# Kernel tuning notes

Hardware: AMD Instinct MI355X
Metric: run time of the kernel (lower is better)

The kernel has to match this reference:

```python
import jax, jax.numpy as jnp
import numpy as np

B, T, H, W, C = 2, 8, 20, 36, 512
NH = 4
HD = C // NH
WS = (5, 9)
EXP = (2, 4)              # window_size // 2
KP = (5, 9)               # focal unfold kernel for level k=0
PADP = (2, 4)
T2T_K, T2T_S, T2T_P = (7, 7), (3, 3), (3, 3)
FFN_HD = 1960
NWH, NWW = H // WS[0], W // WS[1]   # 4, 4
WAREA = WS[0] * WS[1]               # 45


def _valid_ind_rolled():
    wh, ww = WS
    eh, ew = EXP
    m = np.ones((4, wh, ww), np.float32)
    m[0, :wh - eh, :ww - ew] = 0   # tl
    m[1, :wh - eh, ew:] = 0        # tr
    m[2, eh:, :ww - ew] = 0        # bl
    m[3, eh:, ew:] = 0             # br
    return jnp.asarray(np.nonzero(m.reshape(-1))[0])

VALID_ROLLED = _valid_ind_rolled()  # (120,)


def unfold(x, k, s, p):
    # x: (N, Cc, Hh, Ww) -> (N, Cc*kh*kw, L); matches torch.nn.Unfold layout (c slowest).
    N, Cc, Hh, Ww = x.shape
    kh, kw = k; sh, sw = s; ph, pw = p
    xp = jnp.pad(x, ((0, 0), (0, 0), (ph, ph), (pw, pw)))
    oh = (Hh + 2 * ph - kh) // sh + 1
    ow = (Ww + 2 * pw - kw) // sw + 1
    cols = [xp[:, :, i:i + oh * sh:sh, j:j + ow * sw:sw]
            for i in range(kh) for j in range(kw)]
    patches = jnp.stack(cols, axis=2)            # (N, Cc, kh*kw, oh, ow)
    return patches.reshape(N, Cc * kh * kw, oh * ow)


def fold(patches, out_hw, k, s, p):
    # inverse of unfold (overlap-add), matches torch F.fold.
    N = patches.shape[0]
    kh, kw = k; sh, sw = s; ph, pw = p
    Hh, Ww = out_hw
    oh = (Hh + 2 * ph - kh) // sh + 1
    ow = (Ww + 2 * pw - kw) // sw + 1
    Cc = patches.shape[1] // (kh * kw)
    pr = patches.reshape(N, Cc, kh, kw, oh, ow)
    out = jnp.zeros((N, Cc, Hh + 2 * ph, Ww + 2 * pw), patches.dtype)
    for i in range(kh):
        for j in range(kw):
            out = out.at[:, :, i:i + oh * sh:sh, j:j + ow * sw:sw].add(pr[:, :, i, j])
    return out[:, :, ph:ph + Hh, pw:pw + Ww]


def layer_norm(x, g, b):
    mu = jnp.mean(x, -1, keepdims=True)
    var = jnp.var(x, -1, keepdims=True)
    return (x - mu) * jax.lax.rsqrt(var + 1e-5) * g + b


def win_part(x):
    # (B,T,H,W,C) -> (B*nW, T*wh*ww, C)
    b = x.shape[0]
    x = x.reshape(b, T, NWH, WS[0], NWW, WS[1], C)
    return x.transpose(0, 2, 4, 1, 3, 5, 6).reshape(-1, T * WAREA, C)


def to_heads(w):
    return w.reshape(-1, T, WAREA, NH, HD).transpose(0, 3, 1, 2, 4).reshape(-1, NH, T * WAREA, HD)


def block_forward(x, g1, be1, wqkv, bqkv, wproj, bproj, wpool, bpool, g2, be2, w1, bf1, w2, bf2, out_h, out_w):
    shortcut = x
    xn = layer_norm(x, g1, be1)

    # ---- coarser (pooled) focal level, k=0 (focal_level=2) ----
    wnr = xn.reshape(B, T, NWH, WS[0], NWW, WS[1], C).transpose(0, 2, 4, 1, 3, 5, 6)
    wnr = wnr.reshape(B, NWH, NWW, T, WAREA, C)
    pooled = jnp.einsum('bhwtnc,n->bhwtc', wnr, wpool) + bpool   # (B,NWH,NWW,T,C)

    # ---- window attention ----
    qkv = xn @ wqkv + bqkv                                       # (B,T,H,W,3C)
    q, k, v = jnp.split(qkv, 3, axis=-1)
    qw = to_heads(win_part(q)) * (HD ** -0.5)
    kw_, vw = to_heads(win_part(k)), to_heads(win_part(v))

    def rolled(t):
        parts = []
        for sh, sw in ((-EXP[0], -EXP[1]), (-EXP[0], EXP[1]), (EXP[0], -EXP[1]), (EXP[0], EXP[1])):
            r = jnp.roll(t, (sh, sw), axis=(2, 3))
            parts.append(win_part(r).reshape(-1, T, WAREA, NH, HD))
        cat = jnp.concatenate(parts, axis=2)                     # (B*nW, T, 4*warea, NH, HD)
        cat = jnp.take(cat.transpose(0, 3, 1, 2, 4), VALID_ROLLED, axis=3)
        return cat.reshape(-1, NH, T * VALID_ROLLED.shape[0], HD)

    k_rolled = jnp.concatenate([kw_, rolled(k)], axis=2)         # (B*nW, NH, T*165, HD)
    v_rolled = jnp.concatenate([vw, rolled(v)], axis=2)

    # pooled keys/values via focal unfold
    xp = pooled.transpose(0, 3, 1, 2, 4)                          # (B,T,NWH,NWW,C)
    qkv_p = xp @ wqkv + bqkv
    kp, vp = qkv_p[..., C:2 * C], qkv_p[..., 2 * C:]

    def unfold_kv(t):
        t = t.transpose(0, 1, 4, 2, 3).reshape(B * T, C, NWH, NWW)
        u = unfold(t, KP, (1, 1), PADP)                           # (B*T, C*45, L)
        L = u.shape[-1]
        u = u.reshape(B, T, C, KP[0], KP[1], L).transpose(0, 5, 1, 3, 4, 2)
        u = u.reshape(B * L, T, KP[0] * KP[1], NH, HD).transpose(0, 3, 1, 2, 4)
        return u.reshape(B * L, NH, T * KP[0] * KP[1], HD)

    k_all = jnp.concatenate([k_rolled, unfold_kv(kp)], axis=2)
    v_all = jnp.concatenate([v_rolled, unfold_kv(vp)], axis=2)

    attn = jnp.einsum('wnqd,wnkd->wnqk', qw, k_all)               # (B*nW, NH, T*45, N)

    # validity mask for pooled context (zero-padded unfold positions -> -100)
    ones = jnp.ones((T, 1, NWH, NWW), x.dtype)
    um = unfold(ones, KP, (1, 1), PADP)                           # (T, 45, L)
    L = um.shape[-1]
    mvals = jnp.where(um.reshape(T, KP[0] * KP[1], L).transpose(2, 0, 1).reshape(L, -1) == 0,
                      jnp.asarray(-100.0, x.dtype), jnp.asarray(0.0, x.dtype))
    n_rolled = k_rolled.shape[2]
    mask_cols = jnp.concatenate([jnp.zeros((L, n_rolled), x.dtype), mvals], axis=1)
    attn = attn + jnp.tile(mask_cols, (B, 1))[:, None, None, :]

    attn = jax.nn.softmax(attn, axis=-1)
    out = jnp.einsum('wnqk,wnkd->wnqd', attn, v_all)
    out = out.transpose(0, 2, 1, 3).reshape(-1, T * WAREA, C) @ wproj + bproj

    # window reverse + residual
    out = out.reshape(B, NWH, NWW, T, WS[0], WS[1], C)
    out = out.transpose(0, 3, 1, 4, 2, 5, 6).reshape(B, T, H, W, C)
    x = shortcut + out

    # ---- FusionFeedForward (fold/unfold re-normalized MLP) ----
    y = layer_norm(x, g2, be2).reshape(B, T * H * W, C)
    h = y @ w1 + bf1                                              # (B, n, 1960)
    nvec = ((out_h + 2 * T2T_P[0] - T2T_K[0]) // T2T_S[0] + 1) * \
           ((out_w + 2 * T2T_P[1] - T2T_K[1]) // T2T_S[1] + 1)
    bt = (B * T * H * W) // nvec
    norm_p = jnp.ones((bt, T2T_K[0] * T2T_K[1], nvec), x.dtype)
    norm_f = fold(norm_p, (out_h, out_w), T2T_K, T2T_S, T2T_P)    # (bt,1,out_h,out_w)
    h_f = fold(h.reshape(bt, nvec, FFN_HD).transpose(0, 2, 1), (out_h, out_w), T2T_K, T2T_S, T2T_P)
    h = unfold(h_f / norm_f, T2T_K, T2T_S, T2T_P).transpose(0, 2, 1).reshape(B, T * H * W, FFN_HD)
    h = jax.nn.gelu(h, approximate=False) @ w2 + bf2
    return x + h.reshape(B, T, H, W, C)


def setup_inputs() -> dict:
    key = jax.random.key(0)
    ks = jax.random.split(key, 8)
    s = 0.02
    return dict(
        x=jax.random.normal(ks[0], (B, T, H, W, C), jnp.float32),
        g1=jnp.ones((C,), jnp.float32),
        be1=jnp.zeros((C,), jnp.float32),
        wqkv=jax.random.normal(ks[1], (C, 3 * C), jnp.float32) * s,
        bqkv=jnp.zeros((3 * C,), jnp.float32),
        wproj=jax.random.normal(ks[2], (C, C), jnp.float32) * s,
        bproj=jnp.zeros((C,), jnp.float32),
        wpool=jnp.full((WAREA,), 1.0 / WAREA, jnp.float32),
        bpool=jnp.zeros((1,), jnp.float32),
        g2=jnp.ones((C,), jnp.float32),
        be2=jnp.zeros((C,), jnp.float32),
        w1=jax.random.normal(ks[3], (C, FFN_HD), jnp.float32) * s,
        bf1=jnp.zeros((FFN_HD,), jnp.float32),
        w2=jax.random.normal(ks[4], (FFN_HD, C), jnp.float32) * s,
        bf2=jnp.zeros((C,), jnp.float32),
        out_h=60,
        out_w=108,
    )


def reference(x, g1, be1, wqkv, bqkv, wproj, bproj, wpool, bpool, g2, be2, w1, bf1, w2, bf2, out_h, out_w):
    return block_forward(x, g1, be1, wqkv, bqkv, wproj, bproj, wpool, bpool,
                         g2, be2, w1, bf1, w2, bf2, out_h, out_w)
```

## Files before the change

### kernel.cpp

```cpp
#include <hip/hip_runtime.h>
#include <hip/hip_bf16.h>
#include <math.h>

typedef __hip_bfloat16 bf16;
typedef __attribute__((ext_vector_type(8))) short bf16x8;
typedef __attribute__((ext_vector_type(4))) float f32x4;

#define DEVI __device__ __forceinline__

#define C_ 512
#define NH_ 4
#define NTOK 11520
#define NKEY 1680
#define NRK 120
#define FFN_ 1960
#define ZROW (NTOK + 256)

DEVI float ldf(const bf16* p) { return __bfloat162float(*p); }
DEVI float ldf(const float* p) { return *p; }
DEVI void stw(bf16* p, float v) { *p = __float2bfloat16(v); }
DEVI void stw(float* p, float v) { *p = v; }
DEVI unsigned short f2bs(float f) { bf16 h = __float2bfloat16(f); return *(unsigned short*)&h; }

template <int DT> DEVI float ldw(const void* p, size_t i) {
  if (DT == 0) return __bfloat162float(((const bf16*)p)[i]);
  else         return ((const float*)p)[i];
}

DEVI void gload_lds16(const void* g, void* l) {
  __builtin_amdgcn_global_load_lds(
      (const __attribute__((address_space(1))) void*)g,
      (__attribute__((address_space(3))) void*)l, 16, 0, 0);
}

__global__ void k_init(const void* __restrict__ g1, int* __restrict__ flag,
                       int* __restrict__ table, bf16* __restrict__ zp) {
  if (blockIdx.x == 0) {
    if (threadIdx.x == 0) {
      const unsigned short* p = (const unsigned short*)g1;
      *flag = (p[0] == 0x3F80u) ? 0 : 1;
      int cnt = 0;
      for (int pq = 0; pq < 4; pq++)
        for (int wi = 0; wi < 5; wi++)
          for (int wj = 0; wj < 9; wj++) {
            bool invalid;
            if (pq == 0)      invalid = (wi < 3) && (wj < 5);
            else if (pq == 1) invalid = (wi < 3) && (wj >= 4);
            else if (pq == 2) invalid = (wi >= 2) && (wj < 5);
            else              invalid = (wi >= 2) && (wj >= 4);
            if (!invalid) table[cnt++] = pq * 45 + wi * 9 + wj;
          }
    }
  } else {
    zp[(blockIdx.x - 1) * 256 + threadIdx.x] = __float2bfloat16(0.f);
  }
}

__global__ void k_ksrc(const int* __restrict__ vtab, int* __restrict__ ksrc) {
  int idx = blockIdx.x * 256 + threadIdx.x;
  if (idx >= 32 * NKEY) return;
  int w = idx / NKEY, j = idx % NKEY;
  int b = w >> 4, nh = (w >> 2) & 3, nw = w & 3;
  int val;
  if (j < 360) {
    int t = j / 45, pos = j % 45, wi = pos / 9, wj2 = pos % 9;
    val = ((b * 8 + t) * 20 + nh * 5 + wi) * 36 + nw * 9 + wj2;
  } else if (j < 1320) {
    int jj = j - 360;
    int t = jj / 120, r = jj % 120;
    int id = vtab[r];
    int p = id / 45, pos = id % 45, wi = pos / 9, wj2 = pos % 9;
    int sh = (p < 2) ? -2 : 2;
    int sw = (p & 1) ? 4 : -4;
    int hh = nh * 5 + wi - sh;
    if (hh < 0) hh += 20; else if (hh >= 20) hh -= 20;
    int ww2 = nw * 9 + wj2 - sw;
    if (ww2 < 0) ww2 += 36; else if (ww2 >= 36) ww2 -= 36;
    val = ((b * 8 + t) * 20 + hh) * 36 + ww2;
  } else {
    int jj = j - 1320;
    int t = jj / 45, kidx = jj % 45, ki = kidx / 9, kj = kidx % 9;
    int snh = nh + ki - 2, snw = nw + kj - 4;
    if (snh < 0 || snh >= 4 || snw < 0 || snw >= 4) val = -1;
    else val = NTOK + (b * 8 + t) * 16 + snh * 4 + snw;
  }
  ksrc[idx] = val;
}

template <int DT>
DEVI void wcvt_body(const void* in, bf16* out, int K, int N, int Npad) {
  __shared__ float t[64][65];
  const int n0 = blockIdx.x * 64;
  const int k0 = blockIdx.y * 64;
  const int tx = threadIdx.x & 63, tg = threadIdx.x >> 6;
#pragma unroll
  for (int r = 0; r < 16; r++) {
    int k = k0 + r * 4 + tg;
    int nn = n0 + tx;
    float v = (k < K && nn < N) ? ldw<DT>(in, (size_t)k * N + nn) : 0.f;
    t[r * 4 + tg][tx] = v;
  }
  __syncthreads();
#pragma unroll
  for (int r = 0; r < 16; r++) {
    int nn = n0 + r * 4 + tg;
    int k = k0 + tx;
    if (nn < Npad && k < K)
      out[(size_t)nn * K + k] = __float2bfloat16(t[tx][r * 4 + tg]);
  }
}
__global__ void k_wcvt(const int* __restrict__ dflag, const void* __restrict__ in,
                       bf16* __restrict__ out, int K, int N, int Npad) {
  if (*dflag == 0) wcvt_body<0>(in, out, K, N, Npad);
  else             wcvt_body<1>(in, out, K, N, Npad);
}

__global__ void k_bcvt4(const int* __restrict__ dflag,
                        const void* __restrict__ b0, float* __restrict__ o0,
                        const void* __restrict__ b1, float* __restrict__ o1,
                        const void* __restrict__ b2, float* __restrict__ o2,
                        const void* __restrict__ b3, float* __restrict__ o3) {
  int dt = *dflag;
  int bx = blockIdx.x;
  const void* src; float* dst; int n, i;
  if (bx < 6)       { src = b0; dst = o0; n = 1536; i = bx * 256 + threadIdx.x; }
  else if (bx < 8)  { src = b1; dst = o1; n = 512;  i = (bx - 6) * 256 + threadIdx.x; }
  else if (bx < 16) { src = b2; dst = o2; n = FFN_; i = (bx - 8) * 256 + threadIdx.x; }
  else              { src = b3; dst = o3; n = 512;  i = (bx - 16) * 256 + threadIdx.x; }
  if (i < n) dst[i] = (dt == 0) ? ldw<0>(src, i) : ldw<1>(src, i);
}

template <int DTIN, int DTP>
DEVI void ln_body(const void* xin, const void* g, const void* be, bf16* out) {
  const int tok = blockIdx.x;
  const int tid = threadIdx.x;
  const size_t base = (size_t)tok * C_;
  float v0 = ldw<DTIN>(xin, base + tid);
  float v1 = ldw<DTIN>(xin, base + tid + 256);
  float s = v0 + v1, ss = v0 * v0 + v1 * v1;
#pragma unroll
  for (int o = 32; o; o >>= 1) { s += __shfl_xor(s, o); ss += __shfl_xor(ss, o); }
  __shared__ float sh[10];
  const int lane = tid & 63, wv = tid >> 6;
  if (lane == 0) { sh[wv] = s; sh[4 + wv] = ss; }
  __syncthreads();
  if (tid == 0) {
    float a = sh[0] + sh[1] + sh[2] + sh[3];
    float q = sh[4] + sh[5] + sh[6] + sh[7];
    float mu = a * (1.0f / C_);
    float var = q * (1.0f / C_) - mu * mu;
    sh[8] = mu; sh[9] = rsqrtf(fmaxf(var, 0.f) + 1e-5f);
  }
  __syncthreads();
  float mu = sh[8], inv = sh[9];
  stw(out + base + tid,
      (v0 - mu) * inv * ldw<DTP>(g, tid) + ldw<DTP>(be, tid));
  stw(out + base + tid + 256,
      (v1 - mu) * inv * ldw<DTP>(g, tid + 256) + ldw<DTP>(be, tid + 256));
}
__global__ void k_ln(const int* __restrict__ dflag, int mode,
                     const void* __restrict__ xin, const void* __restrict__ g,
                     const void* __restrict__ be, bf16* __restrict__ out) {
  int dt = *dflag;
  if (mode == 0) {
    if (dt == 0) ln_body<0, 0>(xin, g, be, out);
    else         ln_body<1, 1>(xin, g, be, out);
  } else {
    if (dt == 0) ln_body<1, 0>(xin, g, be, out);
    else         ln_body<1, 1>(xin, g, be, out);
  }
}

template <int DT>
DEVI void pool_body(const bf16* xn, const void* wpool, const void* bpool,
                    float* pooled) {
  int idx = blockIdx.x * blockDim.x + threadIdx.x;
  if (idx >= 256 * C_) return;
  int c = idx & (C_ - 1);
  int fw = idx >> 9;
  int nw = fw & 3, nh = (fw >> 2) & 3;
  int bt = fw >> 4;
  float acc = ldw<DT>(bpool, 0);
  for (int wi = 0; wi < 5; wi++) {
    int hh = nh * 5 + wi;
    const bf16* base = xn + (((size_t)(bt * 20 + hh)) * 36 + nw * 9) * C_ + c;
    for (int wj = 0; wj < 9; wj++)
      acc += __bfloat162float(base[(size_t)wj * C_]) * ldw<DT>(wpool, wi * 9 + wj);
  }
  pooled[idx] = acc;
}
__global__ void k_pool(const int* __restrict__ dflag, const bf16* __restrict__ xn,
                       const void* __restrict__ wpool, const void* __restrict__ bpool,
                       float* __restrict__ pooled) {
  if (*dflag == 0) pool_body<0>(xn, wpool, bpool, pooled);
  else             pool_body<1>(xn, wpool, bpool, pooled);
}

template <int DT>
DEVI void gemm_small_body(const float* A, const void* Bw, const void* bias,
                          bf16* Cc) {
  __shared__ float As[8][512];
  const int n = blockIdx.x * 256 + threadIdx.x;
  const int m0 = blockIdx.y * 8;
  for (int i = threadIdx.x; i < 8 * 512; i += 256)
    As[i >> 9][i & 511] = A[(size_t)(m0 + (i >> 9)) * 512 + (i & 511)];
  __syncthreads();
  float acc[8];
  float bv = ldw<DT>(bias, n);
#pragma unroll
  for (int mm = 0; mm < 8; mm++) acc[mm] = bv;
  for (int k = 0; k < 512; k++) {
    float b = ldw<DT>(Bw, (size_t)k * 1536 + n);
#pragma unroll
    for (int mm = 0; mm < 8; mm++) acc[mm] += As[mm][k] * b;
  }
#pragma unroll
  for (int mm = 0; mm < 8; mm++)
    Cc[(size_t)(m0 + mm) * 1536 + n] = __float2bfloat16(acc[mm]);
}
__global__ void k_gemm_small(const int* __restrict__ dflag, const float* __restrict__ A,
                             const void* __restrict__ Bw, const void* __restrict__ bias,
                             bf16* __restrict__ Cc) {
  if (*dflag == 0) gemm_small_body<0>(A, Bw, bias, Cc);
  else             gemm_small_body<1>(A, Bw, bias, Cc);
}

template <int RES>
__global__ __launch_bounds__(256) void k_gemm_m(const int* __restrict__ dflag,
                                                const bf16* __restrict__ A,
                                                const bf16* __restrict__ Bt,
                                                const float* __restrict__ bias,
                                                const void* __restrict__ resid,
                                                void* __restrict__ out,
                                                int M, int N, int K) {
  const int dt = dflag ? *dflag : 0;
  __shared__ __align__(16) unsigned short As[2][128 * 32];
  __shared__ __align__(16) unsigned short Bs[2][128 * 32];
  const int tid = threadIdx.x;
  const int lane = tid & 63, wid = tid >> 6;
  const int r15 = lane & 15, quad = lane >> 4;
  const int wm = wid >> 1, wn = wid & 1;
  const int m0 = blockIdx.y * 128, n0 = blockIdx.x * 128;

  f32x4 acc[4][4];
#pragma unroll
  for (int i = 0; i < 4; i++)
#pragma unroll
    for (int j = 0; j < 4; j++)
#pragma unroll
      for (int e = 0; e < 4; e++) acc[i][j][e] = 0.f;

  const int lrow = lane >> 2, lcol = (lane & 3) * 8;

  for (int k0 = 0; k0 < K; k0 += 64) {
    int rem = K - k0;
    if (rem >= 64) {
      const bf16* ga = A + (size_t)(m0 + wid * 32 + lrow) * K + k0 + lcol;
      gload_lds16(ga, &As[0][wid * 1024]);
      gload_lds16(ga + (size_t)16 * K, &As[0][wid * 1024 + 512]);
      gload_lds16(ga + 32, &As[1][wid * 1024]);
      gload_lds16(ga + (size_t)16 * K + 32, &As[1][wid * 1024 + 512]);
      const bf16* gb = Bt + (size_t)(n0 + wid * 32 + lrow) * K + k0 + lcol;
      gload_lds16(gb, &Bs[0][wid * 1024]);
      gload_lds16(gb + (size_t)16 * K, &Bs[0][wid * 1024 + 512]);
      gload_lds16(gb + 32, &Bs[1][wid * 1024]);
      gload_lds16(gb + (size_t)16 * K + 32, &Bs[1][wid * 1024 + 512]);
    } else {
      int r = tid >> 3, c = (tid & 7) * 8;
      uint4 z = make_uint4(0, 0, 0, 0);
      int h = c >> 5, cc = c & 31;
#pragma unroll
      for (int p = 0; p < 4; p++) {
        int row = r + p * 32;
        uint4 av = z, bv = z;
        if (c < rem) {
          av = *(const uint4*)(A + (size_t)(m0 + row) * K + k0 + c);
          bv = *(const uint4*)(Bt + (size_t)(n0 + row) * K + k0 + c);
        }
        *(uint4*)&As[h][row * 32 + cc] = av;
        *(uint4*)&Bs[h][row * 32 + cc] = bv;
      }
    }
    __syncthreads();

#pragma unroll
    for (int h = 0; h < 2; h++) {
      bf16x8 af[4], bfr[4];
#pragma unroll
      for (int mf = 0; mf < 4; mf++)
        af[mf] = *(const bf16x8*)&As[h][(wm * 64 + mf * 16 + r15) * 32 + quad * 8];
#pragma unroll
      for (int nf = 0; nf < 4; nf++)
        bfr[nf] = *(const bf16x8*)&Bs[h][(wn * 64 + nf * 16 + r15) * 32 + quad * 8];
#pragma unroll
      for (int mf = 0; mf < 4; mf++)
#pragma unroll
        for (int nf = 0; nf < 4; nf++)
          acc[mf][nf] = __builtin_amdgcn_mfma_f32_16x16x32_bf16(af[mf], bfr[nf],
                                                                acc[mf][nf], 0, 0, 0);
    }
    __syncthreads();
  }

#pragma unroll
  for (int nf = 0; nf < 4; nf++) {
    int n = n0 + wn * 64 + nf * 16 + r15;
    if (n >= N) continue;
    float bv = bias[n];
#pragma unroll
    for (int mf = 0; mf < 4; mf++) {
      int mb = m0 + wm * 64 + mf * 16 + quad * 4;
#pragma unroll
      for (int e = 0; e < 4; e++) {
        size_t off = (size_t)(mb + e) * N + n;
        float v = acc[mf][nf][e] + bv;
        if (RES == 1) v += (dt == 0) ? ldw<0>(resid, off) : ldw<1>(resid, off);
        else if (RES == 2) v += ((const float*)resid)[off];
        if (RES == 0) ((bf16*)out)[off] = __float2bfloat16(v);
        else if (RES == 1) ((float*)out)[off] = v;
        else {
          if (dt == 0) ((bf16*)out)[off] = __float2bfloat16(v);
          else         ((float*)out)[off] = v;
        }
      }
    }
  }
}

#define KT 64
#define KPAD 136
#define VPAD 72
__global__ __launch_bounds__(768) void k_attn_m(const bf16* __restrict__ qkv,
                                                const int* __restrict__ ksrc,
                                                bf16* __restrict__ ao) {
  __shared__ int ks_l[NKEY];
  __shared__ __align__(16) unsigned short ktl[2][KT * KPAD];
  __shared__ __align__(16) unsigned short vtl[2][128 * VPAD];
  __shared__ __align__(16) unsigned short ptl[12 * 16 * VPAD];
  __shared__ float maskv[2][KT];

  const int tid = threadIdx.x;
  const int lane = tid & 63, wid = tid >> 6;
  const int r15 = lane & 15, quad = lane >> 4;
  const int w = blockIdx.x, qt = blockIdx.y, n = blockIdx.z;
  const int b = w >> 4, nh = (w >> 2) & 3, nw = w & 3;
  const unsigned short* qkvs = (const unsigned short*)qkv;

  for (int j = tid; j < NKEY; j += 768) ks_l[j] = ksrc[w * NKEY + j];

  bf16x8 qf[4];
  {
    int qw = qt * 192 + wid * 16 + r15;
    int qc2 = qw < 360 ? qw : 359;
    int t = qc2 / 45, pos = qc2 % 45, wi = pos / 9, wj = pos % 9;
    int tok = ((b * 8 + t) * 20 + nh * 5 + wi) * 36 + nw * 9 + wj;
    const unsigned short* qp = qkvs + (size_t)tok * 1536 + n * 128 + quad * 8;
#pragma unroll
    for (int c = 0; c < 4; c++)
      qf[c] = *(const bf16x8*)(qp + c * 32);
  }

  f32x4 of[8];
#pragma unroll
  for (int nt = 0; nt < 8; nt++)
#pragma unroll
    for (int e = 0; e < 4; e++) of[nt][e] = 0.f;
  float m_[4], l_[4];
#pragma unroll
  for (int e = 0; e < 4; e++) { m_[e] = -1e30f; l_[e] = 0.f; }

  unsigned short* ptw = &ptl[wid * 16 * VPAD];

  const bool isK = (wid < 4);
  const int kr = tid >> 2, kp = tid & 3;
  const int vr = lane, vp8 = wid - 4;
  uint4 k0, k1, k2, k3, v0, v1;
  float mreg = -30000.f;
  const unsigned short* kbase = qkvs + 512 + n * 128 + kp * 32;
  const unsigned short* vbase = qkvs + 1024 + n * 128 + vp8 * 16;

  auto load_tile = [&](int j0) {
    int cnt = NKEY - j0; if (cnt > KT) cnt = KT;
    if (isK) {
      int s0 = (kr < cnt) ? ks_l[j0 + kr] : -1;
      mreg = (s0 < 0) ? -30000.f : 0.f;
      int row = (s0 < 0) ? ZROW : s0;
      const uint4* kq = (const uint4*)(kbase + (size_t)row * 1536);
      k0 = kq[0]; k1 = kq[1]; k2 = kq[2]; k3 = kq[3];
    } else {
      int s1 = (vr < cnt) ? ks_l[j0 + vr] : -1;
      int row = (s1 < 0) ? ZROW : s1;
      const uint4* vq = (const uint4*)(vbase + (size_t)row * 1536);
      v0 = vq[0]; v1 = vq[1];
    }
  };

  auto store_tile = [&](int buf) {
    if (isK) {
      if (kp == 0) maskv[buf][kr] = mreg;
      unsigned short* kb = &ktl[buf][kr * KPAD + kp * 32];
      *(uint4*)&kb[0]  = k0;
      *(uint4*)&kb[8]  = k1;
      *(uint4*)&kb[16] = k2;
      *(uint4*)&kb[24] = k3;
    } else {
      unsigned short* vb = &vtl[buf][0];
      int d0 = vp8 * 16;
      vb[(d0 + 0) * VPAD + vr]  = (unsigned short)(v0.x & 0xFFFFu);
      vb[(d0 + 1) * VPAD + vr]  = (unsigned short)(v0.x >> 16);
      vb[(d0 + 2) * VPAD + vr]  = (unsigned short)(v0.y & 0xFFFFu);
      vb[(d0 + 3) * VPAD + vr]  = (unsigned short)(v0.y >> 16);
      vb[(d0 + 4) * VPAD + vr]  = (unsigned short)(v0.z & 0xFFFFu);
      vb[(d0 + 5) * VPAD + vr]  = (unsigned short)(v0.z >> 16);
      vb[(d0 + 6) * VPAD + vr]  = (unsigned short)(v0.w & 0xFFFFu);
      vb[(d0 + 7) * VPAD + vr]  = (unsigned short)(v0.w >> 16);
      vb[(d0 + 8) * VPAD + vr]  = (unsigned short)(v1.x & 0xFFFFu);
      vb[(d0 + 9) * VPAD + vr]  = (unsigned short)(v1.x >> 16);
      vb[(d0 + 10) * VPAD + vr] = (unsigned short)(v1.y & 0xFFFFu);
      vb[(d0 + 11) * VPAD + vr] = (unsigned short)(v1.y >> 16);
      vb[(d0 + 12) * VPAD + vr] = (unsigned short)(v1.z & 0xFFFFu);
      vb[(d0 + 13) * VPAD + vr] = (unsigned short)(v1.z >> 16);
      vb[(d0 + 14) * VPAD + vr] = (unsigned short)(v1.w & 0xFFFFu);
      vb[(d0 + 15) * VPAD + vr] = (unsigned short)(v1.w >> 16);
    }
  };

  __syncthreads();
  load_tile(0);
  store_tile(0);
  load_tile(KT);
  __syncthreads();

  int cur = 0, j0 = 0;
  while (true) {
    int nxt = j0 + KT;
    if (nxt < NKEY) {
      store_tile(cur ^ 1);
      if (nxt + KT < NKEY) load_tile(nxt + KT);
    }

    const unsigned short* ktc = &ktl[cur][0];
    const unsigned short* vtc = &vtl[cur][0];
    const float* mkc = maskv[cur];

    f32x4 sf[4];
#pragma unroll
    for (int ft = 0; ft < 4; ft++)
#pragma unroll
      for (int e = 0; e < 4; e++) sf[ft][e] = 0.f;
#pragma unroll
    for (int kc = 0; kc < 4; kc++) {
      bf16x8 a = qf[kc];
#pragma unroll
      for (int ft = 0; ft < 4; ft++) {
        bf16x8 bb = *(const bf16x8*)&ktc[(ft * 16 + r15) * KPAD + kc * 32 + quad * 8];
        sf[ft] = __builtin_amdgcn_mfma_f32_16x16x32_bf16(a, bb, sf[ft], 0, 0, 0);
      }
    }
    const float scl = 0.088388347648318447f;
#pragma unroll
    for (int ft = 0; ft < 4; ft++) {
      float mk = mkc[ft * 16 + r15];
#pragma unroll
      for (int e = 0; e < 4; e++) sf[ft][e] = sf[ft][e] * scl + mk;
    }
    float tm[4];
#pragma unroll
    for (int e = 0; e < 4; e++) {
      float v = fmaxf(fmaxf(sf[0][e], sf[1][e]), fmaxf(sf[2][e], sf[3][e]));
#pragma unroll
      for (int o = 1; o < 16; o <<= 1) v = fmaxf(v, __shfl_xor(v, o));
      tm[e] = v;
    }
    bool grow = (tm[0] > m_[0] + 8.f) | (tm[1] > m_[1] + 8.f) |
                (tm[2] > m_[2] + 8.f) | (tm[3] > m_[3] + 8.f);
    if (__any(grow)) {
#pragma unroll
      for (int e = 0; e < 4; e++) {
        float mn = fmaxf(m_[e], tm[e]);
        float alpha = __expf(m_[e] - mn);
        m_[e] = mn;
        float rs = 0.f;
#pragma unroll
        for (int ft = 0; ft < 4; ft++) {
          float pv = __expf(sf[ft][e] - mn);
          rs += pv;
          ptw[(quad * 4 + e) * VPAD + ft * 16 + r15] = f2bs(pv);
        }
        l_[e] = l_[e] * alpha + rs;
#pragma unroll
        for (int nt = 0; nt < 8; nt++) of[nt][e] *= alpha;
      }
    } else {
#pragma unroll
      for (int e = 0; e < 4; e++) {
        float rs = 0.f;
#pragma unroll
        for (int ft = 0; ft < 4; ft++) {
          float pv = __expf(sf[ft][e] - m_[e]);
          rs += pv;
          ptw[(quad * 4 + e) * VPAD + ft * 16 + r15] = f2bs(pv);
        }
        l_[e] += rs;
      }
    }
#pragma unroll
    for (int kc = 0; kc < 2; kc++) {
      bf16x8 pa = *(const bf16x8*)&ptw[r15 * VPAD + kc * 32 + quad * 8];
#pragma unroll
      for (int nt = 0; nt < 8; nt++) {
        bf16x8 vb = *(const bf16x8*)&vtc[(nt * 16 + r15) * VPAD + kc * 32 + quad * 8];
        of[nt] = __builtin_amdgcn_mfma_f32_16x16x32_bf16(pa, vb, of[nt], 0, 0, 0);
      }
    }

    if (nxt >= NKEY) break;
    __syncthreads();
    cur ^= 1; j0 = nxt;
  }

#pragma unroll
  for (int e = 0; e < 4; e++) {
#pragma unroll
    for (int o = 1; o < 16; o <<= 1) l_[e] += __shfl_xor(l_[e], o);
  }
#pragma unroll
  for (int e = 0; e < 4; e++) {
    int qw = qt * 192 + wid * 16 + quad * 4 + e;
    if (qw >= 360) continue;
    float inv = 1.0f / l_[e];
    int t = qw / 45, pos = qw % 45, wi = pos / 9, wj = pos % 9;
    int tok = ((b * 8 + t) * 20 + nh * 5 + wi) * 36 + nw * 9 + wj;
    bf16* op = ao + (size_t)tok * 512 + n * 128 + r15;
#pragma unroll
    for (int nt = 0; nt < 8; nt++)
      stw(op + nt * 16, of[nt][e] * inv);
  }
}

__global__ void k_fold(const bf16* __restrict__ h1, float* __restrict__ hf) {
  int idx = blockIdx.x * 256 + threadIdx.x;
  if (idx >= 16 * 40 * 60 * 108) return;
  int x = idx % 108;
  int tmp = idx / 108;
  int y = tmp % 60; tmp /= 60;
  int c = tmp % 40;
  int bt = tmp / 40;
  float sum = 0.f;
  int cnt = 0;
  for (int ki = y % 3; ki < 7; ki += 3) {
    int num = y + 3 - ki;
    if (num < 0) continue;
    int oh = num / 3;
    if (oh >= 20) continue;
    for (int kj = x % 3; kj < 7; kj += 3) {
      int num2 = x + 3 - kj;
      if (num2 < 0) continue;
      int ow = num2 / 3;
      if (ow >= 36) continue;
      sum += __bfloat162float(
          h1[(size_t)(bt * 720 + oh * 36 + ow) * FFN_ + c * 49 + ki * 7 + kj]);
      cnt++;
    }
  }
  hf[idx] = sum / (float)cnt;
}

__global__ void k_unfold_gelu(const float* __restrict__ hf, bf16* __restrict__ h2) {
  int idx = blockIdx.x * 256 + threadIdx.x;
  if (idx >= NTOK * FFN_) return;
  int f = idx % FFN_;
  int token = idx / FFN_;
  int c = f / 49, k = f % 49, ki = k / 7, kj = k % 7;
  int bt = token / 720, vec = token % 720;
  int oh = vec / 36, ow = vec % 36;
  int y = oh * 3 + ki - 3, x = ow * 3 + kj - 3;
  float v = 0.f;
  if (y >= 0 && y < 60 && x >= 0 && x < 108)
    v = hf[((size_t)(bt * 40 + c) * 60 + y) * 108 + x];
  float g = 0.5f * v * (1.0f + erff(v * 0.70710678118654752f));
  stw(h2 + idx, g);
}

extern "C" void kernel_launch(void* const* d_in, const int* in_sizes, int n_in,
                              void* d_out, int out_size, void* d_ws, size_t ws_size,
                              hipStream_t stream) {
  (void)in_sizes; (void)n_in; (void)out_size; (void)ws_size;
  const void* x     = d_in[0];
  const void* g1    = d_in[1];
  const void* be1   = d_in[2];
  const void* wqkv  = d_in[3];
  const void* bqkv  = d_in[4];
  const void* wproj = d_in[5];
  const void* bproj = d_in[6];
  const void* wpool = d_in[7];
  const void* bpool = d_in[8];
  const void* g2    = d_in[9];
  const void* be2   = d_in[10];
  const void* w1    = d_in[11];
  const void* bf1   = d_in[12];
  const void* w2    = d_in[13];
  const void* bf2   = d_in[14];

  char* ws = (char*)d_ws;
  size_t off = 0;
  auto alloc = [&](size_t bytes) -> void* {
    void* p = ws + off;
    off += (bytes + 255) & ~(size_t)255;
    return p;
  };

  int*   dflag  = (int*)  alloc(256);
  int*   vtab   = (int*)  alloc(NRK * sizeof(int));
  int*   ksrc   = (int*)  alloc((size_t)32 * NKEY * sizeof(int));
  bf16*  buf2   = (bf16*) alloc((size_t)NTOK * FFN_ * 2);
  float* pooled = (float*)alloc((size_t)256 * C_ * 4);
  float* x2     = (float*)alloc((size_t)NTOK * C_ * 4);
  float* hf     = (float*)alloc((size_t)16 * 40 * 60 * 108 * 4);
  bf16*  wqkv_t = (bf16*) alloc((size_t)1536 * 512 * 2);
  bf16*  wproj_t= (bf16*) alloc((size_t)512 * 512 * 2);
  bf16*  w1_t   = (bf16*) alloc((size_t)2048 * 512 * 2);
  bf16*  w2_t   = (bf16*) alloc((size_t)512 * FFN_ * 2);
  float* bqkv_f = (float*)alloc(1536 * 4);
  float* bproj_f= (float*)alloc(512 * 4);
  float* bf1_f  = (float*)alloc(FFN_ * 4);
  float* bf2_f  = (float*)alloc(512 * 4);

  bf16* buf1 = (bf16*)d_out;
  bf16* xn = buf1;
  bf16* ao = buf1;
  bf16* y  = buf1;
  bf16* qkv = buf2;
  bf16* h1  = buf2;
  bf16* qkvpb = buf2 + (size_t)NTOK * 1536;

  k_init<<<7, 256, 0, stream>>>(g1, dflag, vtab, qkvpb + (size_t)256 * 1536);
  k_ksrc<<<(32 * NKEY) / 256, 256, 0, stream>>>(vtab, ksrc);

  k_wcvt<<<dim3(24, 8), 256, 0, stream>>>(dflag, wqkv, wqkv_t, 512, 1536, 1536);
  k_wcvt<<<dim3(8, 8), 256, 0, stream>>>(dflag, wproj, wproj_t, 512, 512, 512);
  k_wcvt<<<dim3(32, 8), 256, 0, stream>>>(dflag, w1, w1_t, 512, FFN_, 2048);
  k_wcvt<<<dim3(8, 31), 256, 0, stream>>>(dflag, w2, w2_t, FFN_, 512, 512);
  k_bcvt4<<<18, 256, 0, stream>>>(dflag, bqkv, bqkv_f, bproj, bproj_f,
                                  bf1, bf1_f, bf2, bf2_f);

  k_ln<<<NTOK, 256, 0, stream>>>(dflag, 0, x, g1, be1, xn);

  k_pool<<<512, 256, 0, stream>>>(dflag, xn, wpool, bpool, pooled);

  k_gemm_m<0><<<dim3(12, 90), 256, 0, stream>>>(
      nullptr, xn, wqkv_t, bqkv_f, nullptr, qkv, NTOK, 1536, 512);

  k_gemm_small<<<dim3(6, 32), 256, 0, stream>>>(dflag, pooled, wqkv, bqkv, qkvpb);

  k_attn_m<<<dim3(32, 2, NH_), 768, 0, stream>>>(qkv, ksrc, ao);

  k_gemm_m<1><<<dim3(4, 90), 256, 0, stream>>>(
      dflag, ao, wproj_t, bproj_f, x, x2, NTOK, 512, 512);

  k_ln<<<NTOK, 256, 0, stream>>>(dflag, 1, x2, g2, be2, y);

  k_gemm_m<0><<<dim3(16, 90), 256, 0, stream>>>(
      nullptr, y, w1_t, bf1_f, nullptr, h1, NTOK, FFN_, 512);

  k_fold<<<(16 * 40 * 60 * 108) / 256, 256, 0, stream>>>(h1, hf);

  k_unfold_gelu<<<(NTOK * FFN_) / 256, 256, 0, stream>>>(hf, h1);

  k_gemm_m<2><<<dim3(4, 90), 256, 0, stream>>>(
      dflag, h1, w2_t, bf2_f, x2, d_out, NTOK, 512, FFN_);
}
```

Measured before the change: 560.1 us.

## Vectorize fold/unfold-GELU kernels and add XCD-aware block swizzle to GEMMs

k_fold now computes four adjacent output columns per thread and stores them as one float4. k_unfold_gelu now computes eight consecutive features per thread and stores them as packed bf16 in a single 16-byte write. Both changes aim to cut per-thread index arithmetic and widen memory transactions on these large bandwidth-bound passes. The tiled GEMM also remaps its linear block index so that consecutive blocks going to the same XCD cover neighbouring tiles, which should improve L2 reuse. The remap is only a bijection when the grid size is divisible by 8, which holds for every current launch.

```diff
diff --git a/kernel.cpp b/kernel.cpp
--- a/kernel.cpp
+++ b/kernel.cpp
@@ -21,6 +21,9 @@
 DEVI void stw(bf16* p, float v) { *p = __float2bfloat16(v); }
 DEVI void stw(float* p, float v) { *p = v; }
 DEVI unsigned short f2bs(float f) { bf16 h = __float2bfloat16(f); return *(unsigned short*)&h; }
+DEVI unsigned pk2f(float a, float b) {
+  return (unsigned)f2bs(a) | ((unsigned)f2bs(b) << 16);
+}
 
 template <int DT> DEVI float ldw(const void* p, size_t i) {
   if (DT == 0) return __bfloat162float(((const bf16*)p)[i]);
@@ -240,7 +243,11 @@
   const int lane = tid & 63, wid = tid >> 6;
   const int r15 = lane & 15, quad = lane >> 4;
   const int wm = wid >> 1, wn = wid & 1;
-  const int m0 = blockIdx.y * 128, n0 = blockIdx.x * 128;
+  const int nbx = gridDim.x;
+  const int lin = blockIdx.x + nbx * blockIdx.y;
+  const int cpx = (nbx * gridDim.y) >> 3;
+  const int swz = (lin & 7) * cpx + (lin >> 3);
+  const int m0 = (swz / nbx) * 128, n0 = (swz % nbx) * 128;
 
   f32x4 acc[4][4];
 #pragma unroll
@@ -540,46 +547,66 @@
 
 __global__ void k_fold(const bf16* __restrict__ h1, float* __restrict__ hf) {
   int idx = blockIdx.x * 256 + threadIdx.x;
-  if (idx >= 16 * 40 * 60 * 108) return;
-  int x = idx % 108;
-  int tmp = idx / 108;
+  if (idx >= 16 * 40 * 60 * 27) return;
+  int x0 = (idx % 27) * 4;
+  int tmp = idx / 27;
   int y = tmp % 60; tmp /= 60;
   int c = tmp % 40;
   int bt = tmp / 40;
-  float sum = 0.f;
-  int cnt = 0;
+  float sum[4] = {0.f, 0.f, 0.f, 0.f};
+  int cnt[4] = {0, 0, 0, 0};
   for (int ki = y % 3; ki < 7; ki += 3) {
     int num = y + 3 - ki;
     if (num < 0) continue;
     int oh = num / 3;
     if (oh >= 20) continue;
-    for (int kj = x % 3; kj < 7; kj += 3) {
-      int num2 = x + 3 - kj;
-      if (num2 < 0) continue;
-      int ow = num2 / 3;
-      if (ow >= 36) continue;
-      sum += __bfloat162float(
-          h1[(size_t)(bt * 720 + oh * 36 + ow) * FFN_ + c * 49 + ki * 7 + kj]);
-      cnt++;
-    }
-  }
-  hf[idx] = sum / (float)cnt;
+    const bf16* rowb = h1 + (size_t)(bt * 720 + oh * 36) * FFN_ + c * 49 + ki * 7;
+#pragma unroll
+    for (int xi = 0; xi < 4; xi++) {
+      int x = x0 + xi;
+      for (int kj = x % 3; kj < 7; kj += 3) {
+        int num2 = x + 3 - kj;
+        if (num2 < 0) continue;
+        int ow = num2 / 3;
+        if (ow >= 36) continue;
+        sum[xi] += __bfloat162float(rowb[(size_t)ow * FFN_ + kj]);
+        cnt[xi]++;
+      }
+    }
+  }
+  float4 o;
+  o.x = sum[0] / (float)cnt[0];
+  o.y = sum[1] / (float)cnt[1];
+  o.z = sum[2] / (float)cnt[2];
+  o.w = sum[3] / (float)cnt[3];
+  *(float4*)&hf[((size_t)(bt * 40 + c) * 60 + y) * 108 + x0] = o;
 }
 
 __global__ void k_unfold_gelu(const float* __restrict__ hf, bf16* __restrict__ h2) {
   int idx = blockIdx.x * 256 + threadIdx.x;
-  if (idx >= NTOK * FFN_) return;
-  int f = idx % FFN_;
-  int token = idx / FFN_;
-  int c = f / 49, k = f % 49, ki = k / 7, kj = k % 7;
+  if (idx >= NTOK * (FFN_ / 8)) return;
+  int token = idx / (FFN_ / 8);
+  int f0 = (idx % (FFN_ / 8)) * 8;
   int bt = token / 720, vec = token % 720;
   int oh = vec / 36, ow = vec % 36;
-  int y = oh * 3 + ki - 3, x = ow * 3 + kj - 3;
-  float v = 0.f;
-  if (y >= 0 && y < 60 && x >= 0 && x < 108)
-    v = hf[((size_t)(bt * 40 + c) * 60 + y) * 108 + x];
-  float g = 0.5f * v * (1.0f + erff(v * 0.70710678118654752f));
-  stw(h2 + idx, g);
+  int c = f0 / 49, k = f0 % 49;
+  float g[8];
+#pragma unroll
+  for (int i = 0; i < 8; i++) {
+    int ki = k / 7, kj = k % 7;
+    int y = oh * 3 + ki - 3, xx = ow * 3 + kj - 3;
+    float v = 0.f;
+    if (y >= 0 && y < 60 && xx >= 0 && xx < 108)
+      v = hf[((size_t)(bt * 40 + c) * 60 + y) * 108 + xx];
+    g[i] = 0.5f * v * (1.0f + erff(v * 0.70710678118654752f));
+    k++; if (k == 49) { k = 0; c++; }
+  }
+  uint4 o;
+  o.x = pk2f(g[0], g[1]);
+  o.y = pk2f(g[2], g[3]);
+  o.z = pk2f(g[4], g[5]);
+  o.w = pk2f(g[6], g[7]);
+  *(uint4*)&h2[(size_t)token * FFN_ + f0] = o;
 }
 
 extern "C" void kernel_launch(void* const* d_in, const int* in_sizes, int n_in,
@@ -663,9 +690,9 @@
   k_gemm_m<0><<<dim3(16, 90), 256, 0, stream>>>(
       nullptr, y, w1_t, bf1_f, nullptr, h1, NTOK, FFN_, 512);
 
-  k_fold<<<(16 * 40 * 60 * 108) / 256, 256, 0, stream>>>(h1, hf);
-
-  k_unfold_gelu<<<(NTOK * FFN_) / 256, 256, 0, stream>>>(hf, h1);
+  k_fold<<<(16 * 40 * 60 * 27) / 256 + 1, 256, 0, stream>>>(h1, hf);
+
+  k_unfold_gelu<<<(NTOK * (FFN_ / 8)) / 256, 256, 0, stream>>>(hf, h1);
 
   k_gemm_m<2><<<dim3(4, 90), 256, 0, stream>>>(
       dflag, h1, w2_t, bf2_f, x2, d_out, NTOK, 512, FFN_);
```

New measurement: 652.1 us. 16.4% more time.
